# Kernel optimization log

Hardware: AMD Instinct MI355X
Metric: run time of the kernel (lower is better)

Reference implementation:

```python
import jax, jax.numpy as jnp
import numpy as np

B = 65536
N_SPARSE = 26          # f0..f25, each vocab 5000, embedding dim 1
VOCAB = 5000
N_DENSE = 13
CROSS_VOCAB = VOCAB * VOCAB  # 25_000_000 rows per cross table


def setup_inputs() -> dict:
    key = jax.random.key(0)
    k_dense, k_idx, k_emb, k_c0, k_c1, k_w = jax.random.split(key, 6)
    dense = jax.random.normal(k_dense, (B, N_DENSE), dtype=jnp.float32)
    sparse_idx = jax.random.randint(k_idx, (B, N_SPARSE), 0, VOCAB, dtype=jnp.int64)
    # per-feature dim-1 embedding tables stacked: emb_table[i, v] = weight of feature i, row v
    emb_table = jax.random.normal(k_emb, (N_SPARSE, VOCAB), dtype=jnp.float32) * 0.01
    cross_table0 = jax.random.normal(k_c0, (CROSS_VOCAB,), dtype=jnp.float32) * 0.01
    cross_table1 = jax.random.normal(k_c1, (CROSS_VOCAB,), dtype=jnp.float32) * 0.01
    # Linear(13, 1, bias=False) weight, stored as a [13] vector
    dense_w = jax.random.normal(k_w, (N_DENSE,), dtype=jnp.float32) * 0.1
    return {
        "dense": dense,
        "emb_table": emb_table,
        "cross_table0": cross_table0,
        "cross_table1": cross_table1,
        "dense_w": dense_w,
        "sparse_idx": sparse_idx,
    }


def reference(dense, emb_table, cross_table0, cross_table1, dense_w, sparse_idx):
    # dense arch: Linear(13 -> 1, no bias)  -> [B]
    wide = dense @ dense_w
    # fused multi-table dim-1 gather: vals[b, i] = emb_table[i, sparse_idx[b, i]]
    feat_ids = jnp.arange(N_SPARSE)[None, :]            # [1, 26]
    vals = emb_table[feat_ids, sparse_idx]              # [B, 26]
    wide = wide + vals.sum(axis=1)
    # cross features: idx = f_a * vocab_b + f_b (as in __init__ product)
    c0 = sparse_idx[:, 0] * VOCAB + sparse_idx[:, 1]    # cross_f0_f1
    c1 = sparse_idx[:, 2] * VOCAB + sparse_idx[:, 3]    # cross_f2_f3
    wide = wide + cross_table0[c0] + cross_table1[c1]
    return wide[:, None]                                # [B, 1] like torch Linear output
```

## Files before the change

kernel.cpp:

```cpp
#include <hip/hip_runtime.h>


constexpr int N_DENSE  = 13;
constexpr int N_SPARSE = 26;
constexpr int VOCAB    = 5000;

__global__ __launch_bounds__(256) void wide_fused_kernel(
    const float* __restrict__ dense,
    const float* __restrict__ emb_table,
    const float* __restrict__ cross0,
    const float* __restrict__ cross1,
    const float* __restrict__ dense_w,
    const int*   __restrict__ sparse_idx,
    float*       __restrict__ out,
    int B)
{
    int b = blockIdx.x * blockDim.x + threadIdx.x;
    if (b >= B) return;

    const int* ir = sparse_idx + (size_t)b * N_SPARSE;

    int v0 = ir[0];
    int v1 = ir[1];
    int v2 = ir[2];
    int v3 = ir[3];
    float cr0 = cross0[v0 * VOCAB + v1];
    float cr1 = cross1[v2 * VOCAB + v3];

    float acc = 0.f;
    const float* dr = dense + (size_t)b * N_DENSE;
    #pragma unroll
    for (int j = 0; j < N_DENSE; ++j) acc += dr[j] * dense_w[j];

    acc += emb_table[0 * VOCAB + v0];
    acc += emb_table[1 * VOCAB + v1];
    acc += emb_table[2 * VOCAB + v2];
    acc += emb_table[3 * VOCAB + v3];
    #pragma unroll
    for (int i = 4; i < N_SPARSE; ++i) {
        acc += emb_table[i * VOCAB + ir[i]];
    }

    out[b] = acc + cr0 + cr1;
}

extern "C" void kernel_launch(void* const* d_in, const int* in_sizes, int n_in,
                              void* d_out, int out_size, void* d_ws, size_t ws_size,
                              hipStream_t stream) {
    const float* dense   = (const float*)d_in[0];
    const float* emb     = (const float*)d_in[1];
    const float* cross0  = (const float*)d_in[2];
    const float* cross1  = (const float*)d_in[3];
    const float* dense_w = (const float*)d_in[4];
    const int*   idx     = (const int*)d_in[5];
    float* out = (float*)d_out;

    int B = out_size;
    const int block = 256;
    const int grid  = (B + block - 1) / block;
    wide_fused_kernel<<<grid, block, 0, stream>>>(
        dense, emb, cross0, cross1, dense_w, idx, out, B);
}
```

Before: 189.8 us.

## Split each row across four threads and reduce with wave shuffles

Each batch row is now handled by four adjacent threads. Each thread takes a strided subset of the embedding gathers, dense products and one cross-table lookup, and the partial sums are combined with xor shuffles. This raises the number of threads and loads in flight to hide the latency of the random gathers, and makes the strided index and dense reads closer to coalesced. The cost is four times as many threads, some idle lanes for the cross lookups, and the shuffle reduction overhead.

```diff
diff --git a/kernel.cpp b/kernel.cpp
--- a/kernel.cpp
+++ b/kernel.cpp
@@ -4,6 +4,7 @@
 constexpr int N_DENSE  = 13;
 constexpr int N_SPARSE = 26;
 constexpr int VOCAB    = 5000;
+constexpr int SPLIT    = 4;
 
 __global__ __launch_bounds__(256) void wide_fused_kernel(
     const float* __restrict__ dense,
@@ -15,33 +16,38 @@
     float*       __restrict__ out,
     int B)
 {
-    int b = blockIdx.x * blockDim.x + threadIdx.x;
+    int tid = blockIdx.x * blockDim.x + threadIdx.x;
+    int b = tid >> 2;
+    int s = tid & (SPLIT - 1);
     if (b >= B) return;
 
     const int* ir = sparse_idx + (size_t)b * N_SPARSE;
 
-    int v0 = ir[0];
-    int v1 = ir[1];
-    int v2 = ir[2];
-    int v3 = ir[3];
-    float cr0 = cross0[v0 * VOCAB + v1];
-    float cr1 = cross1[v2 * VOCAB + v3];
+    float acc = 0.f;
 
-    float acc = 0.f;
+    if (s < 2) {
+        int va = ir[2 * s];
+        int vb = ir[2 * s + 1];
+        const float* ct = (s == 0) ? cross0 : cross1;
+        acc += ct[va * VOCAB + vb];
+    }
+
+    #pragma unroll
+    for (int k = 0; k < 7; ++k) {
+        int i = s + SPLIT * k;
+        if (i < N_SPARSE) acc += emb_table[i * VOCAB + ir[i]];
+    }
+
     const float* dr = dense + (size_t)b * N_DENSE;
     #pragma unroll
-    for (int j = 0; j < N_DENSE; ++j) acc += dr[j] * dense_w[j];
-
-    acc += emb_table[0 * VOCAB + v0];
-    acc += emb_table[1 * VOCAB + v1];
-    acc += emb_table[2 * VOCAB + v2];
-    acc += emb_table[3 * VOCAB + v3];
-    #pragma unroll
-    for (int i = 4; i < N_SPARSE; ++i) {
-        acc += emb_table[i * VOCAB + ir[i]];
+    for (int k = 0; k < 4; ++k) {
+        int j = s + SPLIT * k;
+        if (j < N_DENSE) acc += dr[j] * dense_w[j];
     }
 
-    out[b] = acc + cr0 + cr1;
+    acc += __shfl_xor(acc, 1, SPLIT);
+    acc += __shfl_xor(acc, 2, SPLIT);
+    if (s == 0) out[b] = acc;
 }
 
 extern "C" void kernel_launch(void* const* d_in, const int* in_sizes, int n_in,
@@ -57,7 +63,8 @@
 
     int B = out_size;
     const int block = 256;
-    const int grid  = (B + block - 1) / block;
+    const int total = B * SPLIT;
+    const int grid  = (total + block - 1) / block;
     wide_fused_kernel<<<grid, block, 0, stream>>>(
         dense, emb, cross0, cross1, dense_w, idx, out, B);
 }
```

Measured after the change: 192.0 us. Within noise of the previous version (+1.2%).
